# Optimization experiments

Measured on AMD Instinct MI355X. Metric: run time of the kernel, lower is better.

Reference implementation:

```python
import jax, jax.numpy as jnp
import numpy as np

B, V, T, R = 128, 128000, 4096, 64
REP_PENALTY = 1.2   # _rep_penalty (set_repetition_penalty)
MAX_REPS = 3        # _max_reps
REQUIRED_BOOST = 5.0  # _required_boost


def setup_inputs() -> dict:
    key = jax.random.key(0)
    k1, k2, k3, k4 = jax.random.split(key, 4)
    logits = jax.random.normal(k1, (B, V), dtype=jnp.float32)
    generated_so_far = jax.random.randint(k2, (B, T), 0, V, dtype=jnp.int32)
    forbidden_mask = jax.random.bernoulli(k3, 0.01, (V,))
    required_tokens = jax.random.randint(k4, (R,), 0, V, dtype=jnp.int32)
    return {"logits": logits, "generated_so_far": generated_so_far,
            "forbidden_mask": forbidden_mask, "required_tokens": required_tokens}


def reference(logits, generated_so_far, forbidden_mask, required_tokens):
    Bn, Vn = logits.shape
    neg_inf = jnp.float32(-jnp.inf)

    # 1) forbidden tokens -> -inf
    out = jnp.where(forbidden_mask[None, :], neg_inf, logits)

    # per-row token occurrence counts (vectorized bincount) [B, V]
    counts = jnp.zeros((Bn, Vn), jnp.int32).at[
        jnp.arange(Bn)[:, None], generated_so_far
    ].add(1)

    # 2) boost required tokens not yet generated and not forbidden
    present = counts[:, required_tokens] > 0              # [B, R]
    allowed = ~forbidden_mask[required_tokens]            # [R]
    boost = jnp.where((~present) & allowed[None, :],
                      jnp.float32(REQUIRED_BOOST), jnp.float32(0.0))
    out = out.at[:, required_tokens].add(boost)

    # 3) repetition penalty on tokens with count >= MAX_REPS (skip -inf)
    penalized = jnp.where(out > 0, out / REP_PENALTY, out * REP_PENALTY)
    out = jnp.where((counts >= MAX_REPS) & (out != neg_inf), penalized, out)
    return out
```

## Files before the change

### kernel.cpp

```cpp
#include <hip/hip_runtime.h>
#include <cstdint>
#include <cstddef>

#define BB 128
#define VV 128000
#define TT 4096
#define NT 256

#define BSL 4
#define BVR (VV / BSL)
#define BHW (BVR / 4)

typedef float vf4 __attribute__((ext_vector_type(4)));


__device__ __forceinline__ int block_detect(const unsigned char* maskb,
                                            unsigned* det, int tid) {
  if (tid == 0) *det = 0u;
  __syncthreads();
  const uint4* md = (const uint4*)maskb;
  unsigned a = 0u, c = 0u;
#pragma unroll
  for (int k = 0; k < 4; ++k) {
    uint4 w = md[tid + k * NT];
    unsigned o = w.x | w.y | w.z | w.w;
    a |= o & 0x000000FFu;
    c |= o & 0xFFFFFF00u;
  }
  unsigned long long ba = __ballot(a != 0u);
  unsigned long long bc = __ballot(c != 0u);
  if ((tid & 63) == 0) {
    unsigned bits = (ba ? 1u : 0u) | (bc ? 2u : 0u);
    if (bits) atomicOr(det, bits);
  }
  __syncthreads();
  return (*det == 3u) ? 1 : 3;
}

template<int ML>
__global__ __launch_bounds__(NT) void stream_kernel(
    const float* __restrict__ logits,
    const unsigned char* __restrict__ maskb,
    float* __restrict__ out)
{
  int ml = ML;
  if constexpr (ML == -1) {
    __shared__ unsigned det;
    ml = block_detect(maskb, &det, threadIdx.x);
  }
  const float SENT = __uint_as_float(0xFF7F0000u);
  const vf4* lin = (const vf4*)logits;
  vf4*       o4  = (vf4*)out;
  const unsigned* m8  = (const unsigned*)maskb;
  const int4*     m32 = (const int4*)maskb;
  const unsigned totalw = BB * (VV / 4);
  const unsigned stride = gridDim.x * NT;
  for (unsigned i = blockIdx.x * NT + threadIdx.x; i < totalw; i += stride) {
    const unsigned col = i % (unsigned)(VV / 4);
    vf4 x = lin[i];
    unsigned fw;
    if (ml == 1) {
      fw = m8[col];
    } else {
      int4 m = m32[col];
      fw = (m.x ? 1u : 0u) | (m.y ? 0x100u : 0u) |
           (m.z ? 0x10000u : 0u) | (m.w ? 0x1000000u : 0u);
    }
    vf4 r;
#pragma unroll
    for (int j = 0; j < 4; ++j)
      r[j] = ((fw >> (j * 8)) & 0xFFu) ? SENT : x[j];
    o4[i] = r;
  }
}

template<int ML>
__global__ __launch_bounds__(NT) void fixup_kernel(
    const int*  __restrict__ gen,
    const unsigned char* __restrict__ maskb,
    const int*  __restrict__ req,
    float* __restrict__ out,
    int R)
{
  __shared__ unsigned hist[BHW];
  int ml = ML;
  if constexpr (ML == -1) {
    __shared__ unsigned det;
    ml = block_detect(maskb, &det, threadIdx.x);
  }
  const int tid   = threadIdx.x;
  const int b     = blockIdx.x >> 2;
  const int vbase = (blockIdx.x & 3) * BVR;

  for (int i = tid; i < BHW; i += NT) hist[i] = 0u;
  __syncthreads();

  const float RINV = 1.0f / 1.2f;
  auto forb = [&](int t) -> bool {
    if (ml == 1) return maskb[t] != 0;
    return ((const int*)maskb)[t] != 0;
  };

  const int4* grow = (const int4*)(gen + b * TT);
  for (int i = tid; i < TT / 4; i += NT) {
    int4 g = grow[i];
    const int t4[4] = {g.x, g.y, g.z, g.w};
#pragma unroll
    for (int j = 0; j < 4; ++j) {
      const int t = t4[j];
      unsigned d = (unsigned)(t - vbase);
      if (d < (unsigned)BVR) {
        const unsigned sh = (d & 3u) * 8u;
        unsigned old = atomicAdd(&hist[d >> 2], 1u << sh);
        if (((old >> sh) & 0xFFu) == 2u) {
          if (!forb(t)) {
            float* p = out + (size_t)b * VV + t;
            float v = *p;
            *p = (v > 0.0f) ? v * RINV : v * 1.2f;
          }
        }
      }
    }
  }
  __syncthreads();

  for (int r = tid; r < R; r += NT) {
    int t = req[r];
    unsigned d = (unsigned)(t - vbase);
    if (d < (unsigned)BVR) {
      unsigned cnt = (hist[d >> 2] >> ((d & 3u) * 8u)) & 0xFFu;
      if (cnt == 0u && !forb(t))
        atomicAdd(out + (size_t)b * VV + t, 5.0f);
    }
  }
}

extern "C" void kernel_launch(void* const* d_in, const int* in_sizes, int n_in,
                              void* d_out, int out_size, void* d_ws, size_t ws_size,
                              hipStream_t stream) {
  const float* logits = (const float*)d_in[0];
  const int*   gen    = (const int*)d_in[1];
  const unsigned char* maskb = (const unsigned char*)d_in[2];
  const int*   req    = (const int*)d_in[3];
  float* out = (float*)d_out;

  int R = in_sizes[3];
  if (R >= 256 && (R & 3) == 0) R >>= 2;

  int ml;
  if (in_sizes[0] == BB * VV * 4) {
    ml = (in_sizes[2] == VV) ? 1 : 3;
  } else {
    ml = -1;
  }

  const int GA = 2048;
  const int GB = BB * BSL;
  if (ml == 1) {
    stream_kernel<1><<<GA, NT, 0, stream>>>(logits, maskb, out);
    fixup_kernel<1><<<GB, NT, 0, stream>>>(gen, maskb, req, out, R);
  } else if (ml == 3) {
    stream_kernel<3><<<GA, NT, 0, stream>>>(logits, maskb, out);
    fixup_kernel<3><<<GB, NT, 0, stream>>>(gen, maskb, req, out, R);
  } else {
    stream_kernel<-1><<<GA, NT, 0, stream>>>(logits, maskb, out);
    fixup_kernel<-1><<<GB, NT, 0, stream>>>(gen, maskb, req, out, R);
  }
}
```

Baseline: 127.0 us.

## Fuse mask streaming and count fixup into one XCD-aware per-row-slice kernel

Result: faster. 123.9 us (-2.5%).

```diff
diff --git a/kernel.cpp b/kernel.cpp
--- a/kernel.cpp
+++ b/kernel.cpp
@@ -5,11 +5,10 @@
 #define BB 128
 #define VV 128000
 #define TT 4096
+#define SS 16
+#define VR (VV / SS)
+#define HW2 (VR / 4)
 #define NT 256
-
-#define BSL 4
-#define BVR (VV / BSL)
-#define BHW (BVR / 4)
 
 typedef float vf4 __attribute__((ext_vector_type(4)));
 
@@ -38,68 +37,77 @@
 }
 
 template<int ML>
-__global__ __launch_bounds__(NT) void stream_kernel(
+__global__ __launch_bounds__(NT) void enforce_kernel(
     const float* __restrict__ logits,
-    const unsigned char* __restrict__ maskb,
-    float* __restrict__ out)
-{
-  int ml = ML;
-  if constexpr (ML == -1) {
-    __shared__ unsigned det;
-    ml = block_detect(maskb, &det, threadIdx.x);
-  }
-  const float SENT = __uint_as_float(0xFF7F0000u);
-  const vf4* lin = (const vf4*)logits;
-  vf4*       o4  = (vf4*)out;
-  const unsigned* m8  = (const unsigned*)maskb;
-  const int4*     m32 = (const int4*)maskb;
-  const unsigned totalw = BB * (VV / 4);
-  const unsigned stride = gridDim.x * NT;
-  for (unsigned i = blockIdx.x * NT + threadIdx.x; i < totalw; i += stride) {
-    const unsigned col = i % (unsigned)(VV / 4);
-    vf4 x = lin[i];
-    unsigned fw;
-    if (ml == 1) {
-      fw = m8[col];
-    } else {
-      int4 m = m32[col];
-      fw = (m.x ? 1u : 0u) | (m.y ? 0x100u : 0u) |
-           (m.z ? 0x10000u : 0u) | (m.w ? 0x1000000u : 0u);
-    }
-    vf4 r;
-#pragma unroll
-    for (int j = 0; j < 4; ++j)
-      r[j] = ((fw >> (j * 8)) & 0xFFu) ? SENT : x[j];
-    o4[i] = r;
-  }
-}
-
-template<int ML>
-__global__ __launch_bounds__(NT) void fixup_kernel(
     const int*  __restrict__ gen,
     const unsigned char* __restrict__ maskb,
     const int*  __restrict__ req,
     float* __restrict__ out,
     int R)
 {
-  __shared__ unsigned hist[BHW];
+  __shared__ unsigned hist[HW2];
+  __shared__ int cand[64];
+  __shared__ unsigned ncand;
+  const int tid = threadIdx.x;
+
+  const int L    = blockIdx.x;
+  const int xcd  = L & 7;
+  const int q    = L >> 3;
+  const int s    = q & (SS - 1);
+  const int b    = (q >> 4) * 8 + xcd;
+  const int vbase = s * VR;
+
   int ml = ML;
   if constexpr (ML == -1) {
     __shared__ unsigned det;
-    ml = block_detect(maskb, &det, threadIdx.x);
+    ml = block_detect(maskb, &det, tid);
   }
-  const int tid   = threadIdx.x;
-  const int b     = blockIdx.x >> 2;
-  const int vbase = (blockIdx.x & 3) * BVR;
 
-  for (int i = tid; i < BHW; i += NT) hist[i] = 0u;
+  for (int i = tid; i < HW2; i += NT) hist[i] = 0u;
+  if (tid == 0) ncand = 0u;
   __syncthreads();
 
+  const float SENT = __uint_as_float(0xFF7F0000u);
   const float RINV = 1.0f / 1.2f;
-  auto forb = [&](int t) -> bool {
+
+  auto forb1 = [&](int t) -> bool {
     if (ml == 1) return maskb[t] != 0;
     return ((const int*)maskb)[t] != 0;
   };
+
+  const vf4* lrow = (const vf4*)(logits + (size_t)b * VV + vbase);
+  vf4*       orow = (vf4*)(out + (size_t)b * VV + vbase);
+  const unsigned* m8  = (const unsigned*)(maskb + vbase);
+  const int4*     m32 = (const int4*)((const int*)maskb + vbase);
+
+  auto load_mask = [&](int i) -> unsigned {
+    if (ml == 1) return m8[i];
+    int4 m = m32[i];
+    return (m.x ? 1u : 0u) | (m.y ? 0x100u : 0u) |
+           (m.z ? 0x10000u : 0u) | (m.w ? 0x1000000u : 0u);
+  };
+
+  for (int i0 = tid; i0 < HW2; i0 += 2 * NT) {
+    const int i1 = i0 + NT;
+    const bool p1 = (i1 < HW2);
+    vf4 x0 = lrow[i0];
+    unsigned f0 = load_mask(i0);
+    vf4 x1 = {0.f, 0.f, 0.f, 0.f};
+    unsigned f1 = 0u;
+    if (p1) { x1 = lrow[i1]; f1 = load_mask(i1); }
+
+    vf4 r0, r1;
+#pragma unroll
+    for (int j = 0; j < 4; ++j)
+      r0[j] = ((f0 >> (j * 8)) & 0xFFu) ? SENT : x0[j];
+    orow[i0] = r0;
+    if (p1) {
+#pragma unroll
+      for (int j = 0; j < 4; ++j)
+        r1[j] = ((f1 >> (j * 8)) & 0xFFu) ? SENT : x1[j];
+      orow[i1] = r1;
+    }
+  }
 
   const int4* grow = (const int4*)(gen + b * TT);
   for (int i = tid; i < TT / 4; i += NT) {
@@ -109,27 +117,34 @@
     for (int j = 0; j < 4; ++j) {
       const int t = t4[j];
       unsigned d = (unsigned)(t - vbase);
-      if (d < (unsigned)BVR) {
+      if (d < (unsigned)VR) {
         const unsigned sh = (d & 3u) * 8u;
         unsigned old = atomicAdd(&hist[d >> 2], 1u << sh);
         if (((old >> sh) & 0xFFu) == 2u) {
-          if (!forb(t)) {
-            float* p = out + (size_t)b * VV + t;
-            float v = *p;
-            *p = (v > 0.0f) ? v * RINV : v * 1.2f;
-          }
+          unsigned k = atomicAdd(&ncand, 1u);
+          if (k < 64u) cand[k] = t;
         }
       }
     }
   }
   __syncthreads();
 
+  const unsigned nc = ncand < 64u ? ncand : 64u;
+  for (unsigned k = tid; k < nc; k += NT) {
+    const int t = cand[k];
+    if (!forb1(t)) {
+      float* p = out + (size_t)b * VV + t;
+      float v = *p;
+      *p = (v > 0.0f) ? v * RINV : v * 1.2f;
+    }
+  }
+
   for (int r = tid; r < R; r += NT) {
-    int t = req[r];
+    const int t = req[r];
     unsigned d = (unsigned)(t - vbase);
-    if (d < (unsigned)BVR) {
+    if (d < (unsigned)VR) {
       unsigned cnt = (hist[d >> 2] >> ((d & 3u) * 8u)) & 0xFFu;
-      if (cnt == 0u && !forb(t))
+      if (cnt == 0u && !forb1(t))
         atomicAdd(out + (size_t)b * VV + t, 5.0f);
     }
   }
@@ -154,16 +169,8 @@
     ml = -1;
   }
 
-  const int GA = 2048;
-  const int GB = BB * BSL;
-  if (ml == 1) {
-    stream_kernel<1><<<GA, NT, 0, stream>>>(logits, maskb, out);
-    fixup_kernel<1><<<GB, NT, 0, stream>>>(gen, maskb, req, out, R);
-  } else if (ml == 3) {
-    stream_kernel<3><<<GA, NT, 0, stream>>>(logits, maskb, out);
-    fixup_kernel<3><<<GB, NT, 0, stream>>>(gen, maskb, req, out, R);
-  } else {
-    stream_kernel<-1><<<GA, NT, 0, stream>>>(logits, maskb, out);
-    fixup_kernel<-1><<<GB, NT, 0, stream>>>(gen, maskb, req, out, R);
-  }
+  const int G = BB * SS;
+  if (ml == 1)      enforce_kernel<1><<<G, NT, 0, stream>>>(logits, gen, maskb, req, out, R);
+  else if (ml == 3) enforce_kernel<3><<<G, NT, 0, stream>>>(logits, gen, maskb, req, out, R);
+  else              enforce_kernel<-1><<<G, NT, 0, stream>>>(logits, gen, maskb, req, out, R);
 }
```
